# Kernel optimization log

Measured on AMD Instinct MI355X. Metric: run time of the kernel, lower is better.

Reference implementation:

```python
import jax, jax.numpy as jnp
import numpy as np

T, G, D = 64, 1024, 128      # timesteps, detections per timestep, feature dim
N = T * G                    # total points; output rows = 3 + D = 131 cols


def setup_inputs() -> dict:
    key = jax.random.key(0)
    k1, k2 = jax.random.split(key)
    # time column: T distinct timestamps, G detections each (already time-sorted)
    times = jnp.repeat(jnp.arange(T, dtype=jnp.float32), G)
    xy = jax.random.uniform(k1, (N, 2), dtype=jnp.float32) * 128.0
    coor = jnp.concatenate([times[:, None], xy], axis=1)          # [N, 3]
    features = jax.random.normal(k2, (N, D), dtype=jnp.float32)   # [N, 128]
    return {"coor": coor, "features": features, "min_length": 8}


def _traverse(nxt):
    """Greedy chain building with a visited set (faithful to the torch loop).
    nxt[i] = precomputed best cosine match of point i in the next time group
    (-1 if i is in the last group). Returns (out_nodes, cid, clen):
      out_nodes[p] = node emitted at output slot p (all N slots filled),
      cid[p]       = chain id of slot p,
      clen[c]      = length of chain c.
    """
    def chain_cond(carry):
        visited, out, cid, p, cur, length, c = carry
        nx = nxt[cur]
        return (nx >= 0) & (~visited[nx])

    def chain_body(carry):
        visited, out, cid, p, cur, length, c = carry
        nx = nxt[cur]
        visited = visited.at[nx].set(True)
        out = out.at[p].set(nx)
        cid = cid.at[p].set(c)
        return (visited, out, cid, p + 1, nx, length + 1, c)

    def start_chain(st, start):
        visited, out, cid, clen, p, c = st
        visited = visited.at[start].set(True)
        out = out.at[p].set(start)
        cid = cid.at[p].set(c)
        carry = (visited, out, cid, p + 1, start, jnp.int32(1), c)
        visited, out, cid, p, cur, length, _ = jax.lax.while_loop(
            chain_cond, chain_body, carry)
        clen = clen.at[c].set(length)
        return (visited, out, cid, clen, p, c + 1)

    def body(start, st):
        start = jnp.int32(start)
        return jax.lax.cond(st[0][start], lambda s: s,
                            lambda s: start_chain(s, start), st)

    init = (jnp.zeros(N, bool),
            jnp.full(N, -1, jnp.int32),
            jnp.zeros(N, jnp.int32),
            jnp.zeros(N, jnp.int32),
            jnp.int32(0), jnp.int32(0))
    visited, out, cid, clen, p, c = jax.lax.fori_loop(0, N, body, init)
    return out, cid, clen


def reference(coor, features, min_length):
    # sort all points by time (stable; input is already time-sorted)
    order = jnp.argsort(coor[:, 0], stable=True)
    coor = coor[order]
    features = features[order]

    # --- vectorized precompute of the greedy next-match graph ---
    # group points by timestamp: [T, G, D]
    f = features.reshape(T, G, D)
    fn = f / jnp.maximum(jnp.linalg.norm(f, axis=-1, keepdims=True), 1e-6)
    # cosine sims between each time group and the next one: [T-1, G, G]
    sims = jnp.einsum('tgd,thd->tgh', fn[:-1], fn[1:])
    best = jnp.argmax(sims, axis=-1).astype(jnp.int32)        # [T-1, G]
    nxt = jnp.concatenate([
        (jnp.arange(1, T, dtype=jnp.int32)[:, None] * G + best).reshape(-1),
        jnp.full((G,), -1, jnp.int32)])                        # [N]
    nxt = jax.lax.stop_gradient(nxt)

    # --- sequential greedy traversal with visited set ---
    out_nodes, cid, clen = _traverse(nxt)

    # rows = [coor || features] in trajectory order
    rows = jnp.concatenate([coor, features], axis=1)[out_nodes]  # [N, 3+D]
    keep = clen[cid] >= min_length
    # pack kept rows to the top (order preserved), zero-pad the rest
    perm = jnp.argsort(~keep, stable=True)
    return jnp.where(keep[perm][:, None], rows[perm], 0.0)       # [N, 131]
```

## Files before the change

kernel.cpp:

```cpp
#include <hip/hip_runtime.h>
#include <hip/hip_bf16.h>
#include <hip/hip_fp16.h>

#define TT 64
#define GN 1024
#define DK 128
#define NN (TT * GN)
#define OUTC 131
#define TAU 5e-3f

typedef _Float16 f16x8 __attribute__((ext_vector_type(8)));
typedef float    f32x4 __attribute__((ext_vector_type(4)));

__device__ __forceinline__ unsigned f2h(float f) {
    return (unsigned)__half_as_ushort(__float2half(f));
}

__device__ __forceinline__ void gload_lds16(const void* g, void* l) {
    __builtin_amdgcn_global_load_lds(
        (const __attribute__((address_space(1))) unsigned int*)g,
        (__attribute__((address_space(3))) unsigned int*)l, 16, 0, 0);
}

__global__ void kconv(const float* __restrict__ feat, unsigned* __restrict__ fh,
                      float* __restrict__ rnf, double* __restrict__ rnd,
                      int* __restrict__ rcnt, int* __restrict__ clen) {
    if (blockIdx.x == 0 && threadIdx.x < 63) rcnt[threadIdx.x] = 0;
    if (blockIdx.x < 256) clen[blockIdx.x * 256 + threadIdx.x] = 0;
    int row  = blockIdx.x * 4 + (threadIdx.x >> 6);
    int lane = threadIdx.x & 63;
    const float* fr = feat + (size_t)row * DK;
    float2 v = *(const float2*)(fr + lane * 2);
    fh[(size_t)row * 64 + lane] = f2h(v.x) | (f2h(v.y) << 16);
    double s = (double)v.x * (double)v.x + (double)v.y * (double)v.y;
    #pragma unroll
    for (int off = 32; off > 0; off >>= 1)
        s += __shfl_down(s, off);
    if (lane == 0) {
        double m = sqrt(s);
        if (m < 1e-6) m = 1e-6;
        double r = 1.0 / m;
        rnd[row] = r;
        rnf[row] = (float)r;
    }
}

__global__ __launch_bounds__(256) void ksim(const unsigned* __restrict__ fh,
                                            const float* __restrict__ rnf,
                                            unsigned short* __restrict__ nxt16,
                                            int* __restrict__ rcnt,
                                            int* __restrict__ rlistT,
                                            float4* __restrict__ skt) {
    __shared__ int Tiles[2][8192];

    int id = blockIdx.x;
    int t  = id >> 3;
    int mt = id & 7;

    int tid  = threadIdx.x;
    int wave = tid >> 6;
    int lane = tid & 63;
    int la = lane & 15;
    int lq = lane >> 4;
    int wr = (wave & 1) * 64;
    int wc = (wave >> 1) * 64;

    const int* Ag = (const int*)fh + ((size_t)t * GN + mt * 128) * 64;
    const int* Bg = (const int*)fh + (size_t)(t + 1) * GN * 64;

    #pragma unroll
    for (int i = 0; i < 8; ++i) {
        int L = i * 256 + tid;
        int row = L >> 4, colG = (L & 15) ^ (row & 7);
        gload_lds16(Bg + row * 64 + colG * 4, &Tiles[0][L * 4]);
    }

    f16x8 af[4][4];
    #pragma unroll
    for (int kc = 0; kc < 4; ++kc)
        #pragma unroll
        for (int x = 0; x < 4; ++x)
            af[kc][x] = __builtin_bit_cast(f16x8,
                *(const int4*)&Ag[(wr + x * 16 + la) * 64 + (kc * 4 + lq) * 4]);

    float t1[4], t2[4]; int i1[4];
    #pragma unroll
    for (int s = 0; s < 4; ++s) { t1[s] = -3.4e38f; t2[s] = -3.4e38f; i1[s] = 0x7fffffff; }

    const float* rB = rnf + (size_t)(t + 1) * GN;
    __syncthreads();

    #pragma unroll 2
    for (int ntb = 0; ntb < 8; ++ntb) {
        int cur = ntb & 1;
        if (ntb < 7) {
            const int* Bn = Bg + (ntb + 1) * 128 * 64;
            int* dst = Tiles[cur ^ 1];
            #pragma unroll
            for (int i = 0; i < 8; ++i) {
                int L = i * 256 + tid;
                int row = L >> 4, colG = (L & 15) ^ (row & 7);
                gload_lds16(Bn + row * 64 + colG * 4, &dst[L * 4]);
            }
        }

        f32x4 acc[4][4];
        #pragma unroll
        for (int at = 0; at < 4; ++at)
            #pragma unroll
            for (int ct = 0; ct < 4; ++ct) acc[at][ct] = (f32x4){0.f, 0.f, 0.f, 0.f};

        const int* Bt = Tiles[cur];
        #pragma unroll
        for (int kc = 0; kc < 4; ++kc) {
            int sw = ((kc * 4 + lq) ^ (la & 7)) << 2;
            f16x8 bf[4];
            #pragma unroll
            for (int x = 0; x < 4; ++x)
                bf[x] = __builtin_bit_cast(f16x8, *(const int4*)&Bt[(wc + x * 16 + la) * 64 + sw]);
            #pragma unroll
            for (int at = 0; at < 4; ++at)
                #pragma unroll
                for (int ct = 0; ct < 4; ++ct)
                    acc[at][ct] = __builtin_amdgcn_mfma_f32_16x16x32_f16(
                        bf[ct], af[kc][at], acc[at][ct], 0, 0, 0);
        }

        #pragma unroll
        for (int ct = 0; ct < 4; ++ct) {
            float4 rnv = *(const float4*)&rB[ntb * 128 + wc + ct * 16 + lq * 4];
            int nbase = ntb * 128 + wc + ct * 16 + lq * 4;
            float rn[4] = {rnv.x, rnv.y, rnv.z, rnv.w};
            #pragma unroll
            for (int at = 0; at < 4; ++at) {
                #pragma unroll
                for (int reg = 0; reg < 4; ++reg) {
                    float v = acc[at][ct][reg] * rn[reg];
                    t2[at] = fmaxf(t2[at], fminf(v, t1[at]));
                    if (v > t1[at]) { t1[at] = v; i1[at] = nbase + reg; }
                }
            }
        }
        __syncthreads();
    }

    {
        float4* sko = skt + (size_t)((wave >> 1) * 4 + lq) * (63 * GN)
                          + (size_t)t * GN + mt * 128;
        #pragma unroll
        for (int s = 0; s < 4; ++s)
            sko[wr + s * 16 + la] = make_float4(t1[s], t2[s],
                                                __int_as_float(i1[s]), 0.f);
    }

    #pragma unroll
    for (int m = 16; m <= 32; m <<= 1) {
        #pragma unroll
        for (int s = 0; s < 4; ++s) {
            float o1 = __shfl_xor(t1[s], m);
            float o2 = __shfl_xor(t2[s], m);
            int   oi = __shfl_xor(i1[s], m);
            bool take = (o1 > t1[s]) || (o1 == t1[s] && oi < i1[s]);
            float nt2 = take ? fmaxf(o2, t1[s]) : fmaxf(t2[s], o1);
            if (take) { t1[s] = o1; i1[s] = oi; }
            t2[s] = nt2;
        }
    }

    float* mv1 = (float*)Tiles[0];
    float* mv2 = mv1 + 256;
    int*   mi1 = (int*)(mv2 + 256);
    if (lq == 0) {
        #pragma unroll
        for (int s = 0; s < 4; ++s) {
            int row = wr + s * 16 + la;
            int idx = row * 2 + (wave >> 1);
            mv1[idx] = t1[s]; mv2[idx] = t2[s]; mi1[idx] = i1[s];
        }
    }
    __syncthreads();

    if (tid < 128) {
        float best = mv1[tid * 2], sec, bw2 = mv2[tid * 2];
        int bi = mi1[tid * 2];
        float v1 = mv1[tid * 2 + 1], v2 = mv2[tid * 2 + 1];
        int  ii = mi1[tid * 2 + 1];
        if (v1 > best || (v1 == best && ii < bi)) {
            sec = fmaxf(best, v2); best = v1; bi = ii;
        } else {
            sec = fmaxf(v1, bw2);
        }
        int grow = mt * 128 + tid;
        if (best - sec < TAU) {
            int p = atomicAdd(&rcnt[t], 1);
            rlistT[t * 1024 + p] = grow;
        } else {
            nxt16[t * GN + grow] = (unsigned short)bi;
        }
    }
}

__global__ __launch_bounds__(256) void krescue(const float* __restrict__ feat,
                                               const double* __restrict__ rnd,
                                               const int* __restrict__ rcnt,
                                               const int* __restrict__ rlistT,
                                               const float4* __restrict__ skt,
                                               unsigned short* __restrict__ nxt16) {
    int bid = blockIdx.x;
    int t = bid >> 3;
    int nr = rcnt[t];
    if (nr == 0) return;
    int tid  = threadIdx.x;
    int wave = tid >> 6, lane = tid & 63;
    int wk = (bid & 7) * 4 + wave;
    int g  = lane >> 3;
    int o  = (lane & 7) * 16;

    const float*  Bt = feat + (size_t)(t + 1) * GN * DK;
    const double* rb = rnd + (size_t)(t + 1) * GN;

    for (int ri = wk; ri < nr; ri += 32) {
        int arow = rlistT[t * 1024 + ri];

        const float* ar = feat + ((size_t)t * GN + arow) * DK + o;
        double av[16];
        #pragma unroll
        for (int j = 0; j < 16; j += 4) {
            float4 a4 = *(const float4*)(ar + j);
            av[j] = a4.x; av[j + 1] = a4.y; av[j + 2] = a4.z; av[j + 3] = a4.w;
        }

        size_t gb = (size_t)t * GN + arow;
        float4 eg = skt[(size_t)g * (63 * GN) + gb];

        float best = eg.x;
        best = fmaxf(best, __shfl_xor(best, 8));
        best = fmaxf(best, __shfl_xor(best, 16));
        best = fmaxf(best, __shfl_xor(best, 32));
        float thr = best - TAU;

        double bv = -1.0e300; int bi = 0x7fffffff;

        {
            int c = (eg.x >= thr) ? __float_as_int(eg.z) : -1;
            double d = 0.0;
            if (c >= 0) {
                const float* br = Bt + (size_t)c * DK + o;
                #pragma unroll
                for (int j = 0; j < 16; j += 4) {
                    float4 b4 = *(const float4*)(br + j);
                    d = fma(av[j],     (double)b4.x, d);
                    d = fma(av[j + 1], (double)b4.y, d);
                    d = fma(av[j + 2], (double)b4.z, d);
                    d = fma(av[j + 3], (double)b4.w, d);
                }
            }
            d += __shfl_xor(d, 1); d += __shfl_xor(d, 2); d += __shfl_xor(d, 4);
            if (c >= 0) {
                double v = d * rb[c];
                if (v > bv || (v == bv && c < bi)) { bv = v; bi = c; }
            }
        }

        #pragma unroll 1
        for (int s = 0; s < 8; ++s) {
            float ey = __shfl(eg.y, s * 8);
            if (!(ey >= thr)) continue;
            int ch = s >> 2, lqs = s & 3;
            #pragma unroll 1
            for (int r = 0; r < 16; ++r) {
                int j   = r * 8 + g;
                int blk = j >> 2, reg = j & 3;
                int c = (blk >> 2) * 128 + ch * 64 + (blk & 3) * 16 + lqs * 4 + reg;
                const float* br = Bt + (size_t)c * DK + o;
                double d = 0.0;
                #pragma unroll
                for (int jj = 0; jj < 16; jj += 4) {
                    float4 b4 = *(const float4*)(br + jj);
                    d = fma(av[jj],     (double)b4.x, d);
                    d = fma(av[jj + 1], (double)b4.y, d);
                    d = fma(av[jj + 2], (double)b4.z, d);
                    d = fma(av[jj + 3], (double)b4.w, d);
                }
                d += __shfl_xor(d, 1); d += __shfl_xor(d, 2); d += __shfl_xor(d, 4);
                double v = d * rb[c];
                if (v > bv || (v == bv && c < bi)) { bv = v; bi = c; }
            }
        }

        #pragma unroll
        for (int m = 8; m <= 32; m <<= 1) {
            double ov = __shfl_xor(bv, m);
            int    oi = __shfl_xor(bi, m);
            if (ov > bv || (ov == bv && oi < bi)) { bv = ov; bi = oi; }
        }

        if (lane == 0) nxt16[t * GN + arow] = (unsigned short)bi;
    }
}

__global__ __launch_bounds__(1024) void kgraph(const unsigned short* __restrict__ nxt16,
                                               int* __restrict__ chain_of) {
    __shared__ unsigned short ns[64 * 1024];
    __shared__ int winner[2 * GN];
    int g = threadIdx.x;

    #pragma unroll
    for (int i = 0; i < 8; ++i)
        gload_lds16((const char*)nxt16 + ((size_t)i * 1024 + g) * 16,
                    (char*)ns + ((size_t)i * 1024 + g) * 16);

    winner[g] = 0x7fffffff;
    chain_of[g] = g;
    __syncthreads();

    int mychain = g;
    for (int t = 0; t < TT - 1; ++t) {
        int* Wa = winner + (t & 1) * GN;
        int* Wb = winner + ((t + 1) & 1) * GN;
        int j = ns[t * GN + g];
        atomicMin(&Wa[j], mychain);
        Wb[g] = 0x7fffffff;
        __syncthreads();
        int w = Wa[g];
        mychain = (w == 0x7fffffff) ? (((t + 1) << 10) | g) : w;
        ns[t * GN + g] = (unsigned short)mychain;
        __syncthreads();
    }

    for (int t = 0; t < TT - 1; ++t)
        chain_of[(t + 1) * GN + g] = ns[t * GN + g];
}

__global__ void kclen(const int* __restrict__ chain_of, int* __restrict__ clen) {
    int i = blockIdx.x * 256 + threadIdx.x;
    atomicAdd(&clen[chain_of[i]], 1);
}

__global__ __launch_bounds__(1024) void kseg(const int* __restrict__ chain_of,
                                             const int* __restrict__ clen,
                                             const int* __restrict__ minp,
                                             int* __restrict__ oloc,
                                             int* __restrict__ partial) {
    __shared__ int ps[1024];
    int b = blockIdx.x, tid = threadIdx.x;
    int i = b * 1024 + tid;
    int ml = *minp;
    int cl = clen[i];
    int v = (chain_of[i] == i && cl >= ml) ? cl : 0;
    ps[tid] = v;
    __syncthreads();
    for (int off = 1; off < 1024; off <<= 1) {
        int add = (tid >= off) ? ps[tid - off] : 0;
        __syncthreads();
        ps[tid] += add;
        __syncthreads();
    }
    oloc[i] = ps[tid] - v;
    if (tid == 1023) partial[b] = ps[tid];
}

__global__ __launch_bounds__(256) void kout(const float* __restrict__ coor,
                                            const float* __restrict__ feat,
                                            const int* __restrict__ chain_of,
                                            const int* __restrict__ clen,
                                            const int* __restrict__ oloc,
                                            const int* __restrict__ partial,
                                            const int* __restrict__ minp,
                                            float* __restrict__ out) {
    __shared__ int pb[64];
    __shared__ int stot;
    int tid = threadIdx.x;
    if (tid < 64) {
        int v = partial[tid];
        int acc = v;
        #pragma unroll
        for (int off = 1; off < 64; off <<= 1) {
            int o = __shfl_up(acc, off);
            if (tid >= off) acc += o;
        }
        pb[tid] = acc - v;
        if (tid == 63) stot = acc;
    }
    __syncthreads();

    int node = blockIdx.x * 4 + (tid >> 6);
    int lane = tid & 63;
    int s = chain_of[node];
    if (clen[s] >= *minp) {
        int row = oloc[s] + pb[s >> 10] + (node >> 10) - (s >> 10);
        float* orow = out + (size_t)row * OUTC;
        const float* f = feat + (size_t)node * DK;
        if (lane < 3) orow[lane] = coor[(size_t)node * 3 + lane];
        orow[3 + lane]  = f[lane];
        orow[67 + lane] = f[64 + lane];
    }

    int zrow = stot + blockIdx.x * 4 + (tid >> 6);
    if (zrow < NN) {
        float* orow = out + (size_t)zrow * OUTC;
        orow[lane] = 0.f;
        orow[64 + lane] = 0.f;
        if (lane < 3) orow[128 + lane] = 0.f;
    }
}

extern "C" void kernel_launch(void* const* d_in, const int* in_sizes, int n_in,
                              void* d_out, int out_size, void* d_ws, size_t ws_size,
                              hipStream_t stream) {
    const float* coor   = (const float*)d_in[0];
    const float* feat   = (const float*)d_in[1];
    const int*   minlen = (const int*)d_in[2];
    float*       out    = (float*)d_out;

    char* ws = (char*)d_ws;
    double*         rnd      = (double*)(ws);
    float*          rnf      = (float*)(ws + 524288);
    unsigned short* nxt16    = (unsigned short*)(ws + 786432);
    int*            chain_of = (int*)(ws + 917504);
    int*            clen     = (int*)(ws + 1179648);
    int*            oloc     = (int*)(ws + 1441792);
    int*            rcnt     = (int*)(ws + 1703936);
    int*            partial  = (int*)(ws + 1704192);
    int*            rlistT   = (int*)(ws + 1705216);
    unsigned*       fh       = (unsigned*)(ws + 2097152);
    float4*         skt      = (float4*)(ws + 18874368);

    kconv<<<NN / 4, 256, 0, stream>>>(feat, fh, rnf, rnd, rcnt, clen);

    ksim<<<63 * 8, 256, 0, stream>>>(fh, rnf, nxt16, rcnt, rlistT, skt);

    krescue<<<63 * 8, 256, 0, stream>>>(feat, rnd, rcnt, rlistT, skt, nxt16);

    kgraph<<<1, GN, 0, stream>>>(nxt16, chain_of);
    kclen<<<NN / 256, 256, 0, stream>>>(chain_of, clen);
    kseg<<<64, 1024, 0, stream>>>(chain_of, clen, minlen, oloc, partial);
    kout<<<NN / 4, 256, 0, stream>>>(coor, feat, chain_of, clen, oloc, partial,
                                     minlen, out);
}
```

Before: 207.9 us.

## Split ksim across 8 waves and compress rescue candidate records

The similarity kernel now runs 512 threads per block, with each wave covering 32 columns instead of 64. This halves accumulator registers per wave and doubles the waves available to hide latency, and the block merge now combines four column groups. The per-row candidate summary shrinks from float4 to uint2: the second-best value is packed as an fp16 rounded upward together with a 10-bit index, so the summary stays conservative. The rescue kernel is remapped to 16 candidate groups of 4 lanes with 32-element slices to match. Risks are more sync and merge overhead in ksim and a looser rescue threshold that may trigger more fp64 rechecks.

```diff
diff --git a/kernel.cpp b/kernel.cpp
--- a/kernel.cpp
+++ b/kernel.cpp
@@ -14,6 +14,14 @@
 
 __device__ __forceinline__ unsigned f2h(float f) {
     return (unsigned)__half_as_ushort(__float2half(f));
+}
+
+__device__ __forceinline__ unsigned hup(float x) {
+    __half h = __float2half(x);
+    unsigned short b = __half_as_ushort(h);
+    if (__half2float(h) < x)
+        b = (b & 0x8000) ? (unsigned short)(b - 1) : (unsigned short)(b + 1);
+    return (unsigned)b;
 }
 
 __device__ __forceinline__ void gload_lds16(const void* g, void* l) {
@@ -45,12 +53,12 @@
     }
 }
 
-__global__ __launch_bounds__(256) void ksim(const unsigned* __restrict__ fh,
+__global__ __launch_bounds__(512) void ksim(const unsigned* __restrict__ fh,
                                             const float* __restrict__ rnf,
                                             unsigned short* __restrict__ nxt16,
                                             int* __restrict__ rcnt,
                                             int* __restrict__ rlistT,
-                                            float4* __restrict__ skt) {
+                                            uint2* __restrict__ skt) {
     __shared__ int Tiles[2][8192];
 
     int id = blockIdx.x;
@@ -63,14 +71,15 @@
     int la = lane & 15;
     int lq = lane >> 4;
     int wr = (wave & 1) * 64;
-    int wc = (wave >> 1) * 64;
+    int cg = wave >> 1;
+    int wc = cg * 32;
 
     const int* Ag = (const int*)fh + ((size_t)t * GN + mt * 128) * 64;
     const int* Bg = (const int*)fh + (size_t)(t + 1) * GN * 64;
 
     #pragma unroll
-    for (int i = 0; i < 8; ++i) {
-        int L = i * 256 + tid;
+    for (int i = 0; i < 4; ++i) {
+        int L = i * 512 + tid;
         int row = L >> 4, colG = (L & 15) ^ (row & 7);
         gload_lds16(Bg + row * 64 + colG * 4, &Tiles[0][L * 4]);
     }
@@ -97,37 +106,37 @@
             const int* Bn = Bg + (ntb + 1) * 128 * 64;
             int* dst = Tiles[cur ^ 1];
             #pragma unroll
-            for (int i = 0; i < 8; ++i) {
-                int L = i * 256 + tid;
+            for (int i = 0; i < 4; ++i) {
+                int L = i * 512 + tid;
                 int row = L >> 4, colG = (L & 15) ^ (row & 7);
                 gload_lds16(Bn + row * 64 + colG * 4, &dst[L * 4]);
             }
         }
 
-        f32x4 acc[4][4];
+        f32x4 acc[4][2];
         #pragma unroll
         for (int at = 0; at < 4; ++at)
             #pragma unroll
-            for (int ct = 0; ct < 4; ++ct) acc[at][ct] = (f32x4){0.f, 0.f, 0.f, 0.f};
+            for (int ct = 0; ct < 2; ++ct) acc[at][ct] = (f32x4){0.f, 0.f, 0.f, 0.f};
 
         const int* Bt = Tiles[cur];
         #pragma unroll
         for (int kc = 0; kc < 4; ++kc) {
             int sw = ((kc * 4 + lq) ^ (la & 7)) << 2;
-            f16x8 bf[4];
+            f16x8 bf[2];
             #pragma unroll
-            for (int x = 0; x < 4; ++x)
+            for (int x = 0; x < 2; ++x)
                 bf[x] = __builtin_bit_cast(f16x8, *(const int4*)&Bt[(wc + x * 16 + la) * 64 + sw]);
             #pragma unroll
             for (int at = 0; at < 4; ++at)
                 #pragma unroll
-                for (int ct = 0; ct < 4; ++ct)
+                for (int ct = 0; ct < 2; ++ct)
                     acc[at][ct] = __builtin_amdgcn_mfma_f32_16x16x32_f16(
                         bf[ct], af[kc][at], acc[at][ct], 0, 0, 0);
         }
 
         #pragma unroll
-        for (int ct = 0; ct < 4; ++ct) {
+        for (int ct = 0; ct < 2; ++ct) {
             float4 rnv = *(const float4*)&rB[ntb * 128 + wc + ct * 16 + lq * 4];
             int nbase = ntb * 128 + wc + ct * 16 + lq * 4;
             float rn[4] = {rnv.x, rnv.y, rnv.z, rnv.w};
@@ -145,12 +154,12 @@
     }
 
     {
-        float4* sko = skt + (size_t)((wave >> 1) * 4 + lq) * (63 * GN)
-                          + (size_t)t * GN + mt * 128;
+        uint2* sko = skt + (size_t)(cg * 4 + lq) * (63 * GN)
+                         + (size_t)t * GN + mt * 128;
         #pragma unroll
         for (int s = 0; s < 4; ++s)
-            sko[wr + s * 16 + la] = make_float4(t1[s], t2[s],
-                                                __int_as_float(i1[s]), 0.f);
+            sko[wr + s * 16 + la] = make_uint2(__float_as_uint(t1[s]),
+                                               (hup(t2[s]) << 16) | (unsigned)i1[s]);
     }
 
     #pragma unroll
@@ -168,27 +177,30 @@
     }
 
     float* mv1 = (float*)Tiles[0];
-    float* mv2 = mv1 + 256;
-    int*   mi1 = (int*)(mv2 + 256);
+    float* mv2 = mv1 + 512;
+    int*   mi1 = (int*)(mv2 + 512);
     if (lq == 0) {
         #pragma unroll
         for (int s = 0; s < 4; ++s) {
-            int row = wr + s * 16 + la;
-            int idx = row * 2 + (wave >> 1);
+            int idx = (wr + s * 16 + la) * 4 + cg;
             mv1[idx] = t1[s]; mv2[idx] = t2[s]; mi1[idx] = i1[s];
         }
     }
     __syncthreads();
 
     if (tid < 128) {
-        float best = mv1[tid * 2], sec, bw2 = mv2[tid * 2];
-        int bi = mi1[tid * 2];
-        float v1 = mv1[tid * 2 + 1], v2 = mv2[tid * 2 + 1];
-        int  ii = mi1[tid * 2 + 1];
-        if (v1 > best || (v1 == best && ii < bi)) {
-            sec = fmaxf(best, v2); best = v1; bi = ii;
-        } else {
-            sec = fmaxf(v1, bw2);
+        int r4 = tid * 4;
+        float best = mv1[r4], sec = mv2[r4];
+        int bi = mi1[r4];
+        #pragma unroll
+        for (int c = 1; c < 4; ++c) {
+            float v1 = mv1[r4 + c], v2 = mv2[r4 + c];
+            int  ii = mi1[r4 + c];
+            if (v1 > best || (v1 == best && ii < bi)) {
+                sec = fmaxf(sec, fmaxf(best, v2)); best = v1; bi = ii;
+            } else {
+                sec = fmaxf(sec, v1);
+            }
         }
         int grow = mt * 128 + tid;
         if (best - sec < TAU) {
@@ -204,7 +216,7 @@
                                                const double* __restrict__ rnd,
                                                const int* __restrict__ rcnt,
                                                const int* __restrict__ rlistT,
-                                               const float4* __restrict__ skt,
+                                               const uint2* __restrict__ skt,
                                                unsigned short* __restrict__ nxt16) {
     int bid = blockIdx.x;
     int t = bid >> 3;
@@ -213,8 +225,8 @@
     int tid  = threadIdx.x;
     int wave = tid >> 6, lane = tid & 63;
     int wk = (bid & 7) * 4 + wave;
-    int g  = lane >> 3;
-    int o  = (lane & 7) * 16;
+    int g  = lane >> 2;
+    int o  = (lane & 3) * 32;
 
     const float*  Bt = feat + (size_t)(t + 1) * GN * DK;
     const double* rb = rnd + (size_t)(t + 1) * GN;
@@ -223,17 +235,21 @@
         int arow = rlistT[t * 1024 + ri];
 
         const float* ar = feat + ((size_t)t * GN + arow) * DK + o;
-        double av[16];
-        #pragma unroll
-        for (int j = 0; j < 16; j += 4) {
+        double av[32];
+        #pragma unroll
+        for (int j = 0; j < 32; j += 4) {
             float4 a4 = *(const float4*)(ar + j);
             av[j] = a4.x; av[j + 1] = a4.y; av[j + 2] = a4.z; av[j + 3] = a4.w;
         }
 
         size_t gb = (size_t)t * GN + arow;
-        float4 eg = skt[(size_t)g * (63 * GN) + gb];
-
-        float best = eg.x;
+        uint2 eg = skt[(size_t)g * (63 * GN) + gb];
+        float t1  = __uint_as_float(eg.x);
+        float t2u = __half2float(__ushort_as_half((unsigned short)(eg.y >> 16)));
+        int   ic  = (int)(eg.y & 1023u);
+
+        float best = t1;
+        best = fmaxf(best, __shfl_xor(best, 4));
         best = fmaxf(best, __shfl_xor(best, 8));
         best = fmaxf(best, __shfl_xor(best, 16));
         best = fmaxf(best, __shfl_xor(best, 32));
@@ -242,54 +258,54 @@
         double bv = -1.0e300; int bi = 0x7fffffff;
 
         {
-            int c = (eg.x >= thr) ? __float_as_int(eg.z) : -1;
+            int c = (t1 >= thr) ? ic : -1;
             double d = 0.0;
             if (c >= 0) {
                 const float* br = Bt + (size_t)c * DK + o;
                 #pragma unroll
-                for (int j = 0; j < 16; j += 4) {
-                    float4 b4 = *(const float4*)(br + j);
-                    d = fma(av[j],     (double)b4.x, d);
-                    d = fma(av[j + 1], (double)b4.y, d);
-                    d = fma(av[j + 2], (double)b4.z, d);
-                    d = fma(av[j + 3], (double)b4.w, d);
-                }
-            }
-            d += __shfl_xor(d, 1); d += __shfl_xor(d, 2); d += __shfl_xor(d, 4);
-            if (c >= 0) {
-                double v = d * rb[c];
-                if (v > bv || (v == bv && c < bi)) { bv = v; bi = c; }
-            }
-        }
-
-        #pragma unroll 1
-        for (int s = 0; s < 8; ++s) {
-            float ey = __shfl(eg.y, s * 8);
-            if (!(ey >= thr)) continue;
-            int ch = s >> 2, lqs = s & 3;
-            #pragma unroll 1
-            for (int r = 0; r < 16; ++r) {
-                int j   = r * 8 + g;
-                int blk = j >> 2, reg = j & 3;
-                int c = (blk >> 2) * 128 + ch * 64 + (blk & 3) * 16 + lqs * 4 + reg;
-                const float* br = Bt + (size_t)c * DK + o;
-                double d = 0.0;
-                #pragma unroll
-                for (int jj = 0; jj < 16; jj += 4) {
+                for (int jj = 0; jj < 32; jj += 4) {
                     float4 b4 = *(const float4*)(br + jj);
                     d = fma(av[jj],     (double)b4.x, d);
                     d = fma(av[jj + 1], (double)b4.y, d);
                     d = fma(av[jj + 2], (double)b4.z, d);
                     d = fma(av[jj + 3], (double)b4.w, d);
                 }
-                d += __shfl_xor(d, 1); d += __shfl_xor(d, 2); d += __shfl_xor(d, 4);
+            }
+            d += __shfl_xor(d, 1); d += __shfl_xor(d, 2);
+            if (c >= 0) {
                 double v = d * rb[c];
                 if (v > bv || (v == bv && c < bi)) { bv = v; bi = c; }
             }
         }
 
-        #pragma unroll
-        for (int m = 8; m <= 32; m <<= 1) {
+        #pragma unroll 1
+        for (int s = 0; s < 16; ++s) {
+            float ey = __shfl(t2u, s * 4);
+            if (!(ey >= thr)) continue;
+            int cgs = s >> 2, lqs = s & 3;
+            #pragma unroll 1
+            for (int r = 0; r < 4; ++r) {
+                int j = r * 16 + g;
+                int c = (j >> 3) * 128 + cgs * 32 + ((j >> 2) & 1) * 16
+                      + lqs * 4 + (j & 3);
+                const float* br = Bt + (size_t)c * DK + o;
+                double d = 0.0;
+                #pragma unroll
+                for (int jj = 0; jj < 32; jj += 4) {
+                    float4 b4 = *(const float4*)(br + jj);
+                    d = fma(av[jj],     (double)b4.x, d);
+                    d = fma(av[jj + 1], (double)b4.y, d);
+                    d = fma(av[jj + 2], (double)b4.z, d);
+                    d = fma(av[jj + 3], (double)b4.w, d);
+                }
+                d += __shfl_xor(d, 1); d += __shfl_xor(d, 2);
+                double v = d * rb[c];
+                if (v > bv || (v == bv && c < bi)) { bv = v; bi = c; }
+            }
+        }
+
+        #pragma unroll
+        for (int m = 4; m <= 32; m <<= 1) {
             double ov = __shfl_xor(bv, m);
             int    oi = __shfl_xor(bi, m);
             if (ov > bv || (ov == bv && oi < bi)) { bv = ov; bi = oi; }
@@ -424,11 +440,11 @@
     int*            partial  = (int*)(ws + 1704192);
     int*            rlistT   = (int*)(ws + 1705216);
     unsigned*       fh       = (unsigned*)(ws + 2097152);
-    float4*         skt      = (float4*)(ws + 18874368);
+    uint2*          skt      = (uint2*)(ws + 18874368);
 
     kconv<<<NN / 4, 256, 0, stream>>>(feat, fh, rnf, rnd, rcnt, clen);
 
-    ksim<<<63 * 8, 256, 0, stream>>>(fh, rnf, nxt16, rcnt, rlistT, skt);
+    ksim<<<63 * 8, 512, 0, stream>>>(fh, rnf, nxt16, rcnt, rlistT, skt);
 
     krescue<<<63 * 8, 256, 0, stream>>>(feat, rnd, rcnt, rlistT, skt, nxt16);
 
```

Result: faster. 197.9 us (-4.8%).
